# Kernel optimization log

Measured on AMD Instinct MI355X. Metric: run time of the kernel, lower is better.

The kernel has to match this reference:

```python
import jax, jax.numpy as jnp
import numpy as np

LN_EPS = 1e-6  # flax nn.LayerNorm default epsilon
NEG_SLOPE = 0.01  # jax.nn.leaky_relu default


def _layer_norm(x, scale, bias):
    m = jnp.mean(x, axis=-1, keepdims=True)
    v = jnp.mean(jnp.square(x - m), axis=-1, keepdims=True)
    return (x - m) * jax.lax.rsqrt(v + LN_EPS) * scale + bias


def setup_inputs() -> dict:
    key = jax.random.key(0)
    ks = jax.random.split(key, 10)
    B, D1, D2, OUT = 32768, 1024, 512, 1024
    inp = {
        "x1": jax.random.normal(ks[0], (B, D1), dtype=jnp.float32),
        "x2": jax.random.normal(ks[1], (B, D2), dtype=jnp.float32),
        # LayerNorm params (one per stream)
        "ln_scale1": jnp.ones((D1,), jnp.float32),
        "ln_bias1": jnp.zeros((D1,), jnp.float32),
        "ln_scale2": jnp.ones((D2,), jnp.float32),
        "ln_bias2": jnp.zeros((D2,), jnp.float32),
        # output Dense per stream: Dense(output_size)
        "W_out1": jax.random.normal(ks[2], (D1, OUT), jnp.float32) / np.sqrt(D1),
        "b_out1": jnp.zeros((OUT,), jnp.float32),
        "W_out2": jax.random.normal(ks[3], (D2, OUT), jnp.float32) / np.sqrt(D2),
        "b_out2": jnp.zeros((OUT,), jnp.float32),
        # gate Dense per stream: Dense(gate_size=output_size) for POINTWISE
        "W_g1": jax.random.normal(ks[4], (D1, OUT), jnp.float32) / np.sqrt(D1),
        "b_g1": jnp.zeros((OUT,), jnp.float32),
        "W_g2": jax.random.normal(ks[5], (D2, OUT), jnp.float32) / np.sqrt(D2),
        "b_g2": jnp.zeros((OUT,), jnp.float32),
    }
    return inp


def reference(x1, x2, ln_scale1, ln_bias1, ln_scale2, ln_bias2,
              W_out1, b_out1, W_out2, b_out2,
              W_g1, b_g1, W_g2, b_g2):
    # per-stream: LayerNorm -> leaky_relu -> Dense(output_size); pre-Dense
    # activation is also fed to the gate Dense.
    f1 = jax.nn.leaky_relu(_layer_norm(x1, ln_scale1, ln_bias1), NEG_SLOPE)
    f2 = jax.nn.leaky_relu(_layer_norm(x2, ln_scale2, ln_bias2), NEG_SLOPE)
    out1 = f1 @ W_out1 + b_out1  # [B, OUT]
    out2 = f2 @ W_out2 + b_out2  # [B, OUT]
    # two-stream POINTWISE gate: sum of gate Denses, sigmoid; the original
    # broadcasts gate [B,OUT] over stack([out1,out2]) and sums axis 0,
    # i.e. output = gate * (out1 + out2).
    gate = jax.nn.sigmoid((f1 @ W_g1 + b_g1) + (f2 @ W_g2 + b_g2))
    return gate * (out1 + out2)
```

## Files before the change

kernel.cpp:

```cpp
#include <hip/hip_runtime.h>
#include <hip/hip_bf16.h>
#include <stdint.h>

typedef __bf16 bf16x8 __attribute__((ext_vector_type(8)));
typedef float floatx4 __attribute__((ext_vector_type(4)));

__device__ __forceinline__ ushort f2bf(float f) {
  union { float f; uint32_t u; } v; v.f = f;
  uint32_t r = (v.u + 0x7fffu + ((v.u >> 16) & 1u)) >> 16;
  return (ushort)r;
}

__device__ __forceinline__ void load_lds16(const ushort* g, ushort* l) {
  __builtin_amdgcn_global_load_lds(
      (__attribute__((address_space(1))) void*)g,
      (__attribute__((address_space(3))) void*)l, 16, 0, 0);
}

__device__ __forceinline__ float leaky(float x) { return x >= 0.f ? x : 0.01f * x; }

__global__ __launch_bounds__(256) void ln2_kernel(
    const float* __restrict__ x1, const float* __restrict__ x2,
    const float* __restrict__ sc1p, const float* __restrict__ bi1p,
    const float* __restrict__ sc2p, const float* __restrict__ bi2p,
    ushort* __restrict__ f) {
  const int wid = (blockIdx.x << 2) + (threadIdx.x >> 6);
  const int lane = threadIdx.x & 63;

  float4 sc1[4], bi1[4], sc2[2], bi2[2];
#pragma unroll
  for (int j = 0; j < 4; j++) {
    sc1[j] = ((const float4*)sc1p)[j * 64 + lane];
    bi1[j] = ((const float4*)bi1p)[j * 64 + lane];
  }
#pragma unroll
  for (int j = 0; j < 2; j++) {
    sc2[j] = ((const float4*)sc2p)[j * 64 + lane];
    bi2[j] = ((const float4*)bi2p)[j * 64 + lane];
  }

#pragma unroll
  for (int it = 0; it < 2; ++it) {
    const int rA = wid + it * 16384;
    const int rB = rA + 8192;
    const float4* XA1 = (const float4*)(x1 + (size_t)rA * 1024);
    const float4* XA2 = (const float4*)(x2 + (size_t)rA * 512);
    const float4* XB1 = (const float4*)(x1 + (size_t)rB * 1024);
    const float4* XB2 = (const float4*)(x2 + (size_t)rB * 512);
    float4 a1[4], a2[2], b1[4], b2[2];
#pragma unroll
    for (int j = 0; j < 4; j++) a1[j] = XA1[j * 64 + lane];
#pragma unroll
    for (int j = 0; j < 2; j++) a2[j] = XA2[j * 64 + lane];
#pragma unroll
    for (int j = 0; j < 4; j++) b1[j] = XB1[j * 64 + lane];
#pragma unroll
    for (int j = 0; j < 2; j++) b2[j] = XB2[j * 64 + lane];

    float sA1 = 0.f, qA1 = 0.f, sA2 = 0.f, qA2 = 0.f;
    float sB1 = 0.f, qB1 = 0.f, sB2 = 0.f, qB2 = 0.f;
#pragma unroll
    for (int j = 0; j < 4; j++) {
      sA1 += a1[j].x + a1[j].y + a1[j].z + a1[j].w;
      qA1 += a1[j].x * a1[j].x + a1[j].y * a1[j].y + a1[j].z * a1[j].z + a1[j].w * a1[j].w;
      sB1 += b1[j].x + b1[j].y + b1[j].z + b1[j].w;
      qB1 += b1[j].x * b1[j].x + b1[j].y * b1[j].y + b1[j].z * b1[j].z + b1[j].w * b1[j].w;
    }
#pragma unroll
    for (int j = 0; j < 2; j++) {
      sA2 += a2[j].x + a2[j].y + a2[j].z + a2[j].w;
      qA2 += a2[j].x * a2[j].x + a2[j].y * a2[j].y + a2[j].z * a2[j].z + a2[j].w * a2[j].w;
      sB2 += b2[j].x + b2[j].y + b2[j].z + b2[j].w;
      qB2 += b2[j].x * b2[j].x + b2[j].y * b2[j].y + b2[j].z * b2[j].z + b2[j].w * b2[j].w;
    }
#pragma unroll
    for (int o = 1; o < 64; o <<= 1) {
      sA1 += __shfl_xor(sA1, o); qA1 += __shfl_xor(qA1, o);
      sA2 += __shfl_xor(sA2, o); qA2 += __shfl_xor(qA2, o);
      sB1 += __shfl_xor(sB1, o); qB1 += __shfl_xor(qB1, o);
      sB2 += __shfl_xor(sB2, o); qB2 += __shfl_xor(qB2, o);
    }
    const float mA1 = sA1 * (1.0f / 1024.0f);
    const float rA1 = rsqrtf(qA1 * (1.0f / 1024.0f) - mA1 * mA1 + 1e-6f);
    const float mA2 = sA2 * (1.0f / 512.0f);
    const float rA2v = rsqrtf(qA2 * (1.0f / 512.0f) - mA2 * mA2 + 1e-6f);
    const float mB1 = sB1 * (1.0f / 1024.0f);
    const float rB1 = rsqrtf(qB1 * (1.0f / 1024.0f) - mB1 * mB1 + 1e-6f);
    const float mB2 = sB2 * (1.0f / 512.0f);
    const float rB2v = rsqrtf(qB2 * (1.0f / 512.0f) - mB2 * mB2 + 1e-6f);

    ushort* fA = f + (size_t)rA * 1536;
    ushort* fB = f + (size_t)rB * 1536;
#pragma unroll
    for (int j = 0; j < 4; j++) {
      ushort4 oA, oB;
      oA.x = f2bf(leaky((a1[j].x - mA1) * rA1 * sc1[j].x + bi1[j].x));
      oA.y = f2bf(leaky((a1[j].y - mA1) * rA1 * sc1[j].y + bi1[j].y));
      oA.z = f2bf(leaky((a1[j].z - mA1) * rA1 * sc1[j].z + bi1[j].z));
      oA.w = f2bf(leaky((a1[j].w - mA1) * rA1 * sc1[j].w + bi1[j].w));
      oB.x = f2bf(leaky((b1[j].x - mB1) * rB1 * sc1[j].x + bi1[j].x));
      oB.y = f2bf(leaky((b1[j].y - mB1) * rB1 * sc1[j].y + bi1[j].y));
      oB.z = f2bf(leaky((b1[j].z - mB1) * rB1 * sc1[j].z + bi1[j].z));
      oB.w = f2bf(leaky((b1[j].w - mB1) * rB1 * sc1[j].w + bi1[j].w));
      ((ushort4*)fA)[j * 64 + lane] = oA;
      ((ushort4*)fB)[j * 64 + lane] = oB;
    }
#pragma unroll
    for (int j = 0; j < 2; j++) {
      ushort4 oA, oB;
      oA.x = f2bf(leaky((a2[j].x - mA2) * rA2v * sc2[j].x + bi2[j].x));
      oA.y = f2bf(leaky((a2[j].y - mA2) * rA2v * sc2[j].y + bi2[j].y));
      oA.z = f2bf(leaky((a2[j].z - mA2) * rA2v * sc2[j].z + bi2[j].z));
      oA.w = f2bf(leaky((a2[j].w - mA2) * rA2v * sc2[j].w + bi2[j].w));
      oB.x = f2bf(leaky((b2[j].x - mB2) * rB2v * sc2[j].x + bi2[j].x));
      oB.y = f2bf(leaky((b2[j].y - mB2) * rB2v * sc2[j].y + bi2[j].y));
      oB.z = f2bf(leaky((b2[j].z - mB2) * rB2v * sc2[j].z + bi2[j].z));
      oB.w = f2bf(leaky((b2[j].w - mB2) * rB2v * sc2[j].w + bi2[j].w));
      ((ushort4*)(fA + 1024))[j * 64 + lane] = oA;
      ((ushort4*)(fB + 1024))[j * 64 + lane] = oB;
    }
  }
}

__global__ __launch_bounds__(256) void wprep_kernel(
    const float* __restrict__ Wo1, const float* __restrict__ Wo2,
    const float* __restrict__ Wg1, const float* __restrict__ Wg2,
    ushort* __restrict__ WT) {
  __shared__ float tile[32][33];
  const int k0 = blockIdx.x * 32;
  const int j0 = blockIdx.y * 32;
  const int s = blockIdx.z;
  const float* Wa = s ? Wg1 : Wo1;
  const float* Wb = s ? Wg2 : Wo2;
  const int tx = threadIdx.x;
  const int ty = threadIdx.y;
#pragma unroll
  for (int r = 0; r < 4; r++) {
    const int k = k0 + ty + 8 * r;
    const float val = (k < 1024) ? Wa[(size_t)k * 1024 + j0 + tx]
                                 : Wb[(size_t)(k - 1024) * 1024 + j0 + tx];
    tile[ty + 8 * r][tx] = val;
  }
  __syncthreads();
#pragma unroll
  for (int r = 0; r < 4; r++) {
    const int j = j0 + ty + 8 * r;
    const int c = j & 63;
    const int n = (j >> 6) * 128 + (c >> 5) * 64 + s * 32 + ((c >> 4) & 1) * 16 + (c & 15);
    WT[(size_t)n * 1536 + k0 + tx] = f2bf(tile[tx][ty + 8 * r]);
  }
}

__global__ __launch_bounds__(512, 2) void gemm_fused(
    const ushort* __restrict__ A,
    const ushort* __restrict__ Bt,
    const float* __restrict__ bo1, const float* __restrict__ bo2,
    const float* __restrict__ bg1, const float* __restrict__ bg2,
    float* __restrict__ out) {
  __shared__ __align__(16) ushort As[2][16384];
  __shared__ __align__(16) ushort Bs[3][16384];
  const int orig = blockIdx.x;
  const int swz = (orig & 7) * 128 + (orig >> 3);
  const int mt = swz >> 3;
  const int nt = swz & 7;
  const int tid = threadIdx.x;
  const int wave = tid >> 6, lane = tid & 63;
  const int wr = wave >> 2, wcol = wave & 3;
  const int low = lane & 15, quad = lane >> 4;

  const int srow = wave * 8 + (lane >> 3);
  const int schunk = (lane & 7) ^ (lane >> 3);
  const ushort* gA0 = A + ((size_t)mt * 256 + srow) * 1536 + schunk * 8;
  const ushort* gB0 = Bt + ((size_t)nt * 256 + srow) * 1536 + schunk * 8;

  const int q2 = quad ^ (low & 3);
  const int kx = (low >> 2) & 1;
  const int offA_k0 = (wr * 128 + low) * 64 + (q2 + 4 * kx) * 8;
  const int offA_k1 = (wr * 128 + low) * 64 + (q2 + 4 * (1 - kx)) * 8;
  const int offB_k0 = (wcol * 64 + low) * 64 + (q2 + 4 * kx) * 8;
  const int offB_k1 = (wcol * 64 + low) * 64 + (q2 + 4 * (1 - kx)) * 8;

  floatx4 acc[8][4];
#pragma unroll
  for (int m = 0; m < 8; m++)
#pragma unroll
    for (int n = 0; n < 4; n++) acc[m][n] = (floatx4)0.0f;

#define STAGE_A(NB, KT) do { \
    const ushort* s_ = gA0 + (KT) * 64; \
    ushort* d_ = &As[NB][wave * 512]; \
    load_lds16(s_, d_); \
    load_lds16(s_ + 64 * 1536, d_ + 4096); \
    load_lds16(s_ + 128 * 1536, d_ + 8192); \
    load_lds16(s_ + 192 * 1536, d_ + 12288); \
  } while (0)
#define STAGE_B(NB, KT) do { \
    const ushort* s_ = gB0 + (KT) * 64; \
    ushort* d_ = &Bs[NB][wave * 512]; \
    load_lds16(s_, d_); \
    load_lds16(s_ + 64 * 1536, d_ + 4096); \
    load_lds16(s_ + 128 * 1536, d_ + 8192); \
    load_lds16(s_ + 192 * 1536, d_ + 12288); \
  } while (0)

#define MFMA16(MBASE) do { \
    __builtin_amdgcn_s_setprio(1); \
    _Pragma("unroll") for (int m_ = 0; m_ < 4; m_++) \
      _Pragma("unroll") for (int n_ = 0; n_ < 4; n_++) \
        acc[m_ + (MBASE)][n_] = __builtin_amdgcn_mfma_f32_16x16x32_bf16(a[m_], b[n_], acc[m_ + (MBASE)][n_], 0, 0, 0); \
    __builtin_amdgcn_s_setprio(0); \
  } while (0)

  STAGE_A(0, 0);
  STAGE_B(0, 0);
  STAGE_B(1, 1);
  asm volatile("s_waitcnt vmcnt(4)" ::: "memory");
  __builtin_amdgcn_s_barrier();
  asm volatile("" ::: "memory");

#pragma unroll
  for (int t = 0; t < 24; ++t) {
    const ushort* Ac = &As[t & 1][0];
    const ushort* Bc = &Bs[t % 3][0];
    bf16x8 a[4], b[4];
#pragma unroll
    for (int m = 0; m < 4; m++) a[m] = *(const bf16x8*)(Ac + offA_k0 + m * 1024);
#pragma unroll
    for (int n = 0; n < 4; n++) b[n] = *(const bf16x8*)(Bc + offB_k0 + n * 1024);
    if (t < 23) STAGE_A((t + 1) & 1, t + 1);
    asm volatile("" ::: "memory");
    __builtin_amdgcn_s_barrier();
    MFMA16(0);
    asm volatile("" ::: "memory");
    __builtin_amdgcn_s_barrier();
#pragma unroll
    for (int m = 0; m < 4; m++) a[m] = *(const bf16x8*)(Ac + offA_k0 + (m + 4) * 1024);
    if (t < 22) STAGE_B((t + 2) % 3, t + 2);
    asm volatile("" ::: "memory");
    __builtin_amdgcn_s_barrier();
    MFMA16(4);
    asm volatile("" ::: "memory");
    __builtin_amdgcn_s_barrier();
#pragma unroll
    for (int m = 0; m < 4; m++) a[m] = *(const bf16x8*)(Ac + offA_k1 + m * 1024);
#pragma unroll
    for (int n = 0; n < 4; n++) b[n] = *(const bf16x8*)(Bc + offB_k1 + n * 1024);
    asm volatile("" ::: "memory");
    __builtin_amdgcn_s_barrier();
    MFMA16(0);
    asm volatile("" ::: "memory");
    __builtin_amdgcn_s_barrier();
#pragma unroll
    for (int m = 0; m < 4; m++) a[m] = *(const bf16x8*)(Ac + offA_k1 + (m + 4) * 1024);
    asm volatile("" ::: "memory");
    __builtin_amdgcn_s_barrier();
    MFMA16(4);
    if (t < 22) {
      asm volatile("s_waitcnt vmcnt(4)" ::: "memory");
      __builtin_amdgcn_s_barrier();
      asm volatile("" ::: "memory");
    } else if (t == 22) {
      asm volatile("s_waitcnt vmcnt(0)" ::: "memory");
      __builtin_amdgcn_s_barrier();
      asm volatile("" ::: "memory");
    }
  }
#undef MFMA16
#undef STAGE_A
#undef STAGE_B

  const int colbase = (nt * 4 + wcol) << 5;
#pragma unroll
  for (int n = 0; n < 2; n++) {
    const int col = colbase + n * 16 + low;
    const float bs = bo1[col] + bo2[col];
    const float bg = bg1[col] + bg2[col];
#pragma unroll
    for (int m = 0; m < 8; m++) {
      const floatx4 S = acc[m][n];
      const floatx4 G = acc[m][n + 2];
      const size_t rb = (size_t)mt * 256 + wr * 128 + m * 16 + quad * 4;
#pragma unroll
      for (int r = 0; r < 4; r++) {
        const float sv = S[r] + bs;
        const float gv = G[r] + bg;
        const float gate = 1.0f / (1.0f + __expf(-gv));
        out[(rb + r) * 1024 + col] = gate * sv;
      }
    }
  }
}

extern "C" void kernel_launch(void* const* d_in, const int* in_sizes, int n_in,
                              void* d_out, int out_size, void* d_ws, size_t ws_size,
                              hipStream_t stream) {
  const float* x1 = (const float*)d_in[0];
  const float* x2 = (const float*)d_in[1];
  const float* ln_s1 = (const float*)d_in[2];
  const float* ln_b1 = (const float*)d_in[3];
  const float* ln_s2 = (const float*)d_in[4];
  const float* ln_b2 = (const float*)d_in[5];
  const float* W_out1 = (const float*)d_in[6];
  const float* b_out1 = (const float*)d_in[7];
  const float* W_out2 = (const float*)d_in[8];
  const float* b_out2 = (const float*)d_in[9];
  const float* W_g1 = (const float*)d_in[10];
  const float* b_g1 = (const float*)d_in[11];
  const float* W_g2 = (const float*)d_in[12];
  const float* b_g2 = (const float*)d_in[13];
  float* out = (float*)d_out;

  ushort* f = (ushort*)d_ws;
  ushort* WT = f + (size_t)32768 * 1536;

  ln2_kernel<<<2048, 256, 0, stream>>>(x1, x2, ln_s1, ln_b1, ln_s2, ln_b2, f);
  wprep_kernel<<<dim3(48, 32, 2), dim3(32, 8), 0, stream>>>(W_out1, W_out2, W_g1, W_g2, WT);
  gemm_fused<<<dim3(1024), dim3(512), 0, stream>>>(f, WT, b_out1, b_out2, b_g1, b_g2, out);
}
```

Baseline: 519.1 us.

## Simplify GEMM pipeline to plain double buffering with one barrier per k-step

Replaces the triple-buffered B and staggered A/B staging, which used several barriers per k-tile, with a simple double buffer for both operands. The next A and B tiles are issued at the top of each iteration, and there is a single vmcnt(0) wait and barrier at the end. This cuts barrier overhead and shrinks LDS use. In exchange, each iteration waits for all loads to finish, so memory latency is less hidden and MFMA work from different waves no longer interleaves. The main loop is also no longer fully unrolled.

```diff
diff --git a/kernel.cpp b/kernel.cpp
--- a/kernel.cpp
+++ b/kernel.cpp
@@ -158,7 +158,7 @@
     const float* __restrict__ bg1, const float* __restrict__ bg2,
     float* __restrict__ out) {
   __shared__ __align__(16) ushort As[2][16384];
-  __shared__ __align__(16) ushort Bs[3][16384];
+  __shared__ __align__(16) ushort Bs[2][16384];
   const int orig = blockIdx.x;
   const int swz = (orig & 7) * 128 + (orig >> 3);
   const int mt = swz >> 3;
@@ -186,23 +186,6 @@
 #pragma unroll
     for (int n = 0; n < 4; n++) acc[m][n] = (floatx4)0.0f;
 
-#define STAGE_A(NB, KT) do { \
-    const ushort* s_ = gA0 + (KT) * 64; \
-    ushort* d_ = &As[NB][wave * 512]; \
-    load_lds16(s_, d_); \
-    load_lds16(s_ + 64 * 1536, d_ + 4096); \
-    load_lds16(s_ + 128 * 1536, d_ + 8192); \
-    load_lds16(s_ + 192 * 1536, d_ + 12288); \
-  } while (0)
-#define STAGE_B(NB, KT) do { \
-    const ushort* s_ = gB0 + (KT) * 64; \
-    ushort* d_ = &Bs[NB][wave * 512]; \
-    load_lds16(s_, d_); \
-    load_lds16(s_ + 64 * 1536, d_ + 4096); \
-    load_lds16(s_ + 128 * 1536, d_ + 8192); \
-    load_lds16(s_ + 192 * 1536, d_ + 12288); \
-  } while (0)
-
 #define MFMA16(MBASE) do { \
     __builtin_amdgcn_s_setprio(1); \
     _Pragma("unroll") for (int m_ = 0; m_ < 4; m_++) \
@@ -211,63 +194,62 @@
     __builtin_amdgcn_s_setprio(0); \
   } while (0)
 
-  STAGE_A(0, 0);
-  STAGE_B(0, 0);
-  STAGE_B(1, 1);
-  asm volatile("s_waitcnt vmcnt(4)" ::: "memory");
+  {
+    ushort* dA = &As[0][wave * 512];
+    ushort* dB = &Bs[0][wave * 512];
+    load_lds16(gA0, dA);
+    load_lds16(gA0 + 64 * 1536, dA + 4096);
+    load_lds16(gA0 + 128 * 1536, dA + 8192);
+    load_lds16(gA0 + 192 * 1536, dA + 12288);
+    load_lds16(gB0, dB);
+    load_lds16(gB0 + 64 * 1536, dB + 4096);
+    load_lds16(gB0 + 128 * 1536, dB + 8192);
+    load_lds16(gB0 + 192 * 1536, dB + 12288);
+  }
+  asm volatile("s_waitcnt vmcnt(0)" ::: "memory");
   __builtin_amdgcn_s_barrier();
   asm volatile("" ::: "memory");
 
-#pragma unroll
   for (int t = 0; t < 24; ++t) {
-    const ushort* Ac = &As[t & 1][0];
-    const ushort* Bc = &Bs[t % 3][0];
+    const int cur = t & 1;
+    const ushort* Ac = (const ushort*)As + cur * 16384;
+    const ushort* Bc = (const ushort*)Bs + cur * 16384;
+    if (t < 23) {
+      ushort* dA = (ushort*)As + (cur ^ 1) * 16384 + wave * 512;
+      ushort* dB = (ushort*)Bs + (cur ^ 1) * 16384 + wave * 512;
+      const ushort* sA = gA0 + (t + 1) * 64;
+      const ushort* sB = gB0 + (t + 1) * 64;
+      load_lds16(sA, dA);
+      load_lds16(sA + 64 * 1536, dA + 4096);
+      load_lds16(sA + 128 * 1536, dA + 8192);
+      load_lds16(sA + 192 * 1536, dA + 12288);
+      load_lds16(sB, dB);
+      load_lds16(sB + 64 * 1536, dB + 4096);
+      load_lds16(sB + 128 * 1536, dB + 8192);
+      load_lds16(sB + 192 * 1536, dB + 12288);
+    }
     bf16x8 a[4], b[4];
 #pragma unroll
     for (int m = 0; m < 4; m++) a[m] = *(const bf16x8*)(Ac + offA_k0 + m * 1024);
 #pragma unroll
     for (int n = 0; n < 4; n++) b[n] = *(const bf16x8*)(Bc + offB_k0 + n * 1024);
-    if (t < 23) STAGE_A((t + 1) & 1, t + 1);
+    MFMA16(0);
+#pragma unroll
+    for (int m = 0; m < 4; m++) a[m] = *(const bf16x8*)(Ac + offA_k0 + (m + 4) * 1024);
+    MFMA16(4);
+#pragma unroll
+    for (int m = 0; m < 4; m++) a[m] = *(const bf16x8*)(Ac + offA_k1 + m * 1024);
+#pragma unroll
+    for (int n = 0; n < 4; n++) b[n] = *(const bf16x8*)(Bc + offB_k1 + n * 1024);
+    MFMA16(0);
+#pragma unroll
+    for (int m = 0; m < 4; m++) a[m] = *(const bf16x8*)(Ac + offA_k1 + (m + 4) * 1024);
+    MFMA16(4);
+    asm volatile("s_waitcnt vmcnt(0)" ::: "memory");
+    __builtin_amdgcn_s_barrier();
     asm volatile("" ::: "memory");
-    __builtin_amdgcn_s_barrier();
-    MFMA16(0);
-    asm volatile("" ::: "memory");
-    __builtin_amdgcn_s_barrier();
-#pragma unroll
-    for (int m = 0; m < 4; m++) a[m] = *(const bf16x8*)(Ac + offA_k0 + (m + 4) * 1024);
-    if (t < 22) STAGE_B((t + 2) % 3, t + 2);
-    asm volatile("" ::: "memory");
-    __builtin_amdgcn_s_barrier();
-    MFMA16(4);
-    asm volatile("" ::: "memory");
-    __builtin_amdgcn_s_barrier();
-#pragma unroll
-    for (int m = 0; m < 4; m++) a[m] = *(const bf16x8*)(Ac + offA_k1 + m * 1024);
-#pragma unroll
-    for (int n = 0; n < 4; n++) b[n] = *(const bf16x8*)(Bc + offB_k1 + n * 1024);
-    asm volatile("" ::: "memory");
-    __builtin_amdgcn_s_barrier();
-    MFMA16(0);
-    asm volatile("" ::: "memory");
-    __builtin_amdgcn_s_barrier();
-#pragma unroll
-    for (int m = 0; m < 4; m++) a[m] = *(const bf16x8*)(Ac + offA_k1 + (m + 4) * 1024);
-    asm volatile("" ::: "memory");
-    __builtin_amdgcn_s_barrier();
-    MFMA16(4);
-    if (t < 22) {
-      asm volatile("s_waitcnt vmcnt(4)" ::: "memory");
-      __builtin_amdgcn_s_barrier();
-      asm volatile("" ::: "memory");
-    } else if (t == 22) {
-      asm volatile("s_waitcnt vmcnt(0)" ::: "memory");
-      __builtin_amdgcn_s_barrier();
-      asm volatile("" ::: "memory");
-    }
   }
 #undef MFMA16
-#undef STAGE_A
-#undef STAGE_B
 
   const int colbase = (nt * 4 + wcol) << 5;
 #pragma unroll
```

New measurement: 541.1 us. 4.2% more time.

## Shrink GEMM tile to 128x128 with 4 waves and simple double buffering

Applied to the files above, without the earlier changes.

Changes the fused GEMM from 256x256 tiles with 8 waves and a triple-buffered B pipeline to 128x128 tiles with 4 waves, double-buffered A and B, and a full vmcnt(0) wait each K step. The grid becomes 4096 blocks with a new swizzle. The goal is more blocks per CU and more parallelism. In exchange, each tile reuses data less, so global and L2 traffic roughly doubles, and the pipeline is shallower, which can expose load latency.

```diff
diff --git a/kernel.cpp b/kernel.cpp
--- a/kernel.cpp
+++ b/kernel.cpp
@@ -151,135 +151,114 @@
   }
 }
 
-__global__ __launch_bounds__(512, 2) void gemm_fused(
+__global__ __launch_bounds__(256, 2) void gemm_fused(
     const ushort* __restrict__ A,
     const ushort* __restrict__ Bt,
     const float* __restrict__ bo1, const float* __restrict__ bo2,
     const float* __restrict__ bg1, const float* __restrict__ bg2,
     float* __restrict__ out) {
-  __shared__ __align__(16) ushort As[2][16384];
-  __shared__ __align__(16) ushort Bs[3][16384];
+  __shared__ __align__(16) ushort As[2][8192];
+  __shared__ __align__(16) ushort Bs[2][8192];
   const int orig = blockIdx.x;
-  const int swz = (orig & 7) * 128 + (orig >> 3);
-  const int mt = swz >> 3;
-  const int nt = swz & 7;
+  const int swz = (orig & 7) * 512 + (orig >> 3);
+  const int mt = swz >> 4;
+  const int nt = swz & 15;
   const int tid = threadIdx.x;
   const int wave = tid >> 6, lane = tid & 63;
-  const int wr = wave >> 2, wcol = wave & 3;
+  const int wr = wave >> 1, wc = wave & 1;
   const int low = lane & 15, quad = lane >> 4;
 
-  const int srow = wave * 8 + (lane >> 3);
-  const int schunk = (lane & 7) ^ (lane >> 3);
-  const ushort* gA0 = A + ((size_t)mt * 256 + srow) * 1536 + schunk * 8;
-  const ushort* gB0 = Bt + ((size_t)nt * 256 + srow) * 1536 + schunk * 8;
+  const int row_local = tid >> 3;
+  const int schunk = (tid & 7) ^ (row_local & 7);
+  const ushort* gA0 = A + ((size_t)mt * 128 + row_local) * 1536 + schunk * 8;
+  const ushort* gB0 = Bt + ((size_t)nt * 128 + row_local) * 1536 + schunk * 8;
 
   const int q2 = quad ^ (low & 3);
   const int kx = (low >> 2) & 1;
-  const int offA_k0 = (wr * 128 + low) * 64 + (q2 + 4 * kx) * 8;
-  const int offA_k1 = (wr * 128 + low) * 64 + (q2 + 4 * (1 - kx)) * 8;
-  const int offB_k0 = (wcol * 64 + low) * 64 + (q2 + 4 * kx) * 8;
-  const int offB_k1 = (wcol * 64 + low) * 64 + (q2 + 4 * (1 - kx)) * 8;
-
-  floatx4 acc[8][4];
-#pragma unroll
-  for (int m = 0; m < 8; m++)
+  const int offA_k0 = (wr * 64 + low) * 64 + (q2 + 4 * kx) * 8;
+  const int offA_k1 = (wr * 64 + low) * 64 + (q2 + 4 * (1 - kx)) * 8;
+  const int offB_k0 = (wc * 64 + low) * 64 + (q2 + 4 * kx) * 8;
+  const int offB_k1 = (wc * 64 + low) * 64 + (q2 + 4 * (1 - kx)) * 8;
+
+  floatx4 acc[4][4];
+#pragma unroll
+  for (int m = 0; m < 4; m++)
 #pragma unroll
     for (int n = 0; n < 4; n++) acc[m][n] = (floatx4)0.0f;
 
-#define STAGE_A(NB, KT) do { \
+#define STAGE_A(BUF, KT) do { \
     const ushort* s_ = gA0 + (KT) * 64; \
-    ushort* d_ = &As[NB][wave * 512]; \
+    ushort* d_ = &As[BUF][wave * 512]; \
     load_lds16(s_, d_); \
+    load_lds16(s_ + 32 * 1536, d_ + 2048); \
     load_lds16(s_ + 64 * 1536, d_ + 4096); \
-    load_lds16(s_ + 128 * 1536, d_ + 8192); \
-    load_lds16(s_ + 192 * 1536, d_ + 12288); \
+    load_lds16(s_ + 96 * 1536, d_ + 6144); \
   } while (0)
-#define STAGE_B(NB, KT) do { \
+#define STAGE_B(BUF, KT) do { \
     const ushort* s_ = gB0 + (KT) * 64; \
-    ushort* d_ = &Bs[NB][wave * 512]; \
+    ushort* d_ = &Bs[BUF][wave * 512]; \
     load_lds16(s_, d_); \
+    load_lds16(s_ + 32 * 1536, d_ + 2048); \
     load_lds16(s_ + 64 * 1536, d_ + 4096); \
-    load_lds16(s_ + 128 * 1536, d_ + 8192); \
-    load_lds16(s_ + 192 * 1536, d_ + 12288); \
+    load_lds16(s_ + 96 * 1536, d_ + 6144); \
   } while (0)
 
-#define MFMA16(MBASE) do { \
+#define MFMA16() do { \
     __builtin_amdgcn_s_setprio(1); \
     _Pragma("unroll") for (int m_ = 0; m_ < 4; m_++) \
       _Pragma("unroll") for (int n_ = 0; n_ < 4; n_++) \
-        acc[m_ + (MBASE)][n_] = __builtin_amdgcn_mfma_f32_16x16x32_bf16(a[m_], b[n_], acc[m_ + (MBASE)][n_], 0, 0, 0); \
+        acc[m_][n_] = __builtin_amdgcn_mfma_f32_16x16x32_bf16(a[m_], b[n_], acc[m_][n_], 0, 0, 0); \
     __builtin_amdgcn_s_setprio(0); \
   } while (0)
 
   STAGE_A(0, 0);
   STAGE_B(0, 0);
-  STAGE_B(1, 1);
-  asm volatile("s_waitcnt vmcnt(4)" ::: "memory");
+  asm volatile("s_waitcnt vmcnt(0)" ::: "memory");
   __builtin_amdgcn_s_barrier();
   asm volatile("" ::: "memory");
 
-#pragma unroll
   for (int t = 0; t < 24; ++t) {
-    const ushort* Ac = &As[t & 1][0];
-    const ushort* Bc = &Bs[t % 3][0];
+    const int cur = t & 1;
+    const ushort* Ac = (const ushort*)As + cur * 8192;
+    const ushort* Bc = (const ushort*)Bs + cur * 8192;
     bf16x8 a[4], b[4];
 #pragma unroll
     for (int m = 0; m < 4; m++) a[m] = *(const bf16x8*)(Ac + offA_k0 + m * 1024);
 #pragma unroll
     for (int n = 0; n < 4; n++) b[n] = *(const bf16x8*)(Bc + offB_k0 + n * 1024);
-    if (t < 23) STAGE_A((t + 1) & 1, t + 1);
-    asm volatile("" ::: "memory");
-    __builtin_amdgcn_s_barrier();
-    MFMA16(0);
-    asm volatile("" ::: "memory");
-    __builtin_amdgcn_s_barrier();
-#pragma unroll
-    for (int m = 0; m < 4; m++) a[m] = *(const bf16x8*)(Ac + offA_k0 + (m + 4) * 1024);
-    if (t < 22) STAGE_B((t + 2) % 3, t + 2);
-    asm volatile("" ::: "memory");
-    __builtin_amdgcn_s_barrier();
-    MFMA16(4);
+    if (t < 23) STAGE_A(cur ^ 1, t + 1);
+    asm volatile("" ::: "memory");
+    __builtin_amdgcn_s_barrier();
+    MFMA16();
     asm volatile("" ::: "memory");
     __builtin_amdgcn_s_barrier();
 #pragma unroll
     for (int m = 0; m < 4; m++) a[m] = *(const bf16x8*)(Ac + offA_k1 + m * 1024);
 #pragma unroll
     for (int n = 0; n < 4; n++) b[n] = *(const bf16x8*)(Bc + offB_k1 + n * 1024);
-    asm volatile("" ::: "memory");
-    __builtin_amdgcn_s_barrier();
-    MFMA16(0);
-    asm volatile("" ::: "memory");
-    __builtin_amdgcn_s_barrier();
-#pragma unroll
-    for (int m = 0; m < 4; m++) a[m] = *(const bf16x8*)(Ac + offA_k1 + (m + 4) * 1024);
-    asm volatile("" ::: "memory");
-    __builtin_amdgcn_s_barrier();
-    MFMA16(4);
-    if (t < 22) {
-      asm volatile("s_waitcnt vmcnt(4)" ::: "memory");
-      __builtin_amdgcn_s_barrier();
-      asm volatile("" ::: "memory");
-    } else if (t == 22) {
-      asm volatile("s_waitcnt vmcnt(0)" ::: "memory");
-      __builtin_amdgcn_s_barrier();
-      asm volatile("" ::: "memory");
-    }
+    if (t < 23) STAGE_B(cur ^ 1, t + 1);
+    asm volatile("" ::: "memory");
+    __builtin_amdgcn_s_barrier();
+    MFMA16();
+    asm volatile("s_waitcnt vmcnt(0)" ::: "memory");
+    __builtin_amdgcn_s_barrier();
+    asm volatile("" ::: "memory");
   }
 #undef MFMA16
 #undef STAGE_A
 #undef STAGE_B
 
-  const int colbase = (nt * 4 + wcol) << 5;
+  const int colbase = nt * 64 + wc * 32;
 #pragma unroll
   for (int n = 0; n < 2; n++) {
     const int col = colbase + n * 16 + low;
     const float bs = bo1[col] + bo2[col];
     const float bg = bg1[col] + bg2[col];
 #pragma unroll
-    for (int m = 0; m < 8; m++) {
+    for (int m = 0; m < 4; m++) {
       const floatx4 S = acc[m][n];
       const floatx4 G = acc[m][n + 2];
-      const size_t rb = (size_t)mt * 256 + wr * 128 + m * 16 + quad * 4;
+      const size_t rb = (size_t)mt * 128 + wr * 64 + m * 16 + quad * 4;
 #pragma unroll
       for (int r = 0; r < 4; r++) {
         const float sv = S[r] + bs;
@@ -315,5 +294,5 @@
 
   ln2_kernel<<<2048, 256, 0, stream>>>(x1, x2, ln_s1, ln_b1, ln_s2, ln_b2, f);
   wprep_kernel<<<dim3(48, 32, 2), dim3(32, 8), 0, stream>>>(W_out1, W_out2, W_g1, W_g2, WT);
-  gemm_fused<<<dim3(1024), dim3(512), 0, stream>>>(f, WT, b_out1, b_out2, b_g1, b_g2, out);
-}
+  gemm_fused<<<dim3(4096), dim3(256), 0, stream>>>(f, WT, b_out1, b_out2, b_g1, b_g2, out);
+}
```

Result: slower. 575.1 us (+10.8%).
